# Kernel optimization log

Measured on AMD Instinct MI355X. Metric: run time of the kernel, lower is better.

Reference implementation:

```python
import jax, jax.numpy as jnp
import numpy as np

A_DIM = 18
HID = 512
LSTM_IN = HID + A_DIM + 1  # 531


def setup_inputs() -> dict:
    key = jax.random.key(0)
    ks = jax.random.split(key, 26)
    T, B = 80, 64
    inp = {}
    inp["o"] = jax.random.randint(ks[0], (T, B, 1, 84, 84), 0, 255, dtype=jnp.int32)
    inp["a"] = jax.random.randint(ks[1], (T, B), 0, A_DIM, dtype=jnp.int32)
    inp["r"] = jax.random.normal(ks[2], (T, B), dtype=jnp.float32)
    inp["done"] = jax.random.randint(ks[3], (T, B), 0, 2, dtype=jnp.int32)
    inp["h0"] = jnp.zeros((B, HID), dtype=jnp.float32)
    inp["c0"] = jnp.zeros((B, HID), dtype=jnp.float32)

    def gw(k, shape, s=0.05):
        return (jax.random.normal(k, shape, dtype=jnp.float32) * s)

    # CNN trunk params (torch Conv2d OIHW layout)
    inp["conv1_w"] = gw(ks[4], (32, 1, 8, 8))
    inp["conv1_b"] = jnp.zeros((32,), jnp.float32)
    inp["conv2_w"] = gw(ks[5], (64, 32, 4, 4))
    inp["conv2_b"] = jnp.zeros((64,), jnp.float32)
    inp["conv3_w"] = gw(ks[6], (64, 64, 3, 3))
    inp["conv3_b"] = jnp.zeros((64,), jnp.float32)
    inp["fc_w"] = gw(ks[7], (HID, 64 * 7 * 7))
    inp["fc_b"] = jnp.zeros((HID,), jnp.float32)
    # LSTM params (torch gate order: i, f, g, o)
    inp["W_ih"] = gw(ks[8], (4 * HID, LSTM_IN))
    inp["W_hh"] = gw(ks[9], (4 * HID, HID))
    inp["b_ih"] = jnp.zeros((4 * HID,), jnp.float32)
    inp["b_hh"] = jnp.zeros((4 * HID,), jnp.float32)
    # Dueling heads
    inp["adv_w1"] = gw(ks[10], (HID, HID))
    inp["adv_b1"] = jnp.zeros((HID,), jnp.float32)
    inp["adv_w2"] = gw(ks[11], (A_DIM, HID))
    inp["adv_b2"] = jnp.zeros((A_DIM,), jnp.float32)
    inp["val_w1"] = gw(ks[12], (HID, HID))
    inp["val_b1"] = jnp.zeros((HID,), jnp.float32)
    inp["val_w2"] = gw(ks[13], (1, HID))
    inp["val_b2"] = jnp.zeros((1,), jnp.float32)
    return inp


def _conv(x, w, b, stride):
    y = jax.lax.conv_general_dilated(
        x, w, (stride, stride), 'VALID',
        dimension_numbers=('NCHW', 'OIHW', 'NCHW'))
    return y + b[None, :, None, None]


def reference(o, a, r, done, h0, c0,
              conv1_w, conv1_b, conv2_w, conv2_b, conv3_w, conv3_b,
              fc_w, fc_b, W_ih, W_hh, b_ih, b_hh,
              adv_w1, adv_b1, adv_w2, adv_b2,
              val_w1, val_b1, val_w2, val_b2):
    T, B = o.shape[0], o.shape[1]
    x = o.reshape(T * B, 1, 84, 84).astype(jnp.float32) / 255.0
    x = jax.nn.relu(_conv(x, conv1_w, conv1_b, 4))   # [TB,32,20,20]
    x = jax.nn.relu(_conv(x, conv2_w, conv2_b, 2))   # [TB,64,9,9]
    x = jax.nn.relu(_conv(x, conv3_w, conv3_b, 1))   # [TB,64,7,7]
    x = x.reshape(T * B, 64 * 7 * 7)
    hidden = jax.nn.relu(x @ fc_w.T + fc_b).reshape(T, B, HID)

    a_one_hot = jax.nn.one_hot(a, A_DIM, dtype=jnp.float32)      # [T,B,A]
    lstm_in = jnp.concatenate([hidden, r[..., None], a_one_hot], axis=-1)  # [T,B,531]
    keep = (1.0 - done.astype(jnp.float32))[..., None]           # [T,B,1]
    bias = b_ih + b_hh

    def step(carry, inp_t):
        h, c = carry
        x_t, m = inp_t
        h = h * m
        c = c * m
        g = x_t @ W_ih.T + h @ W_hh.T + bias   # [B, 4H]
        i, f, gg, oo = jnp.split(g, 4, axis=-1)
        c = jax.nn.sigmoid(f) * c + jax.nn.sigmoid(i) * jnp.tanh(gg)
        h = jax.nn.sigmoid(oo) * jnp.tanh(c)
        return (h, c), h

    (hT, cT), hs = jax.lax.scan(step, (h0, c0), (lstm_in, keep))
    z = hs.reshape(T * B, HID)

    adv = jax.nn.relu(z @ adv_w1.T + adv_b1) @ adv_w2.T + adv_b2  # [TB,A]
    val = jax.nn.relu(z @ val_w1.T + val_b1) @ val_w2.T + val_b2  # [TB,1]
    q = val + (adv - adv.mean(axis=1, keepdims=True))
    return q.reshape(T, B, A_DIM), hT, cT
```

## Files before the change

### kernel.cpp

```cpp
#include <hip/hip_runtime.h>
#include <hip/hip_bf16.h>
#include <stdint.h>

typedef __bf16 bf16;
typedef __bf16 bfrag __attribute__((ext_vector_type(8)));
typedef short s16x8 __attribute__((ext_vector_type(8)));
typedef float f32x4 __attribute__((ext_vector_type(4)));
typedef float f32x16 __attribute__((ext_vector_type(16)));
typedef uint32_t u32x4 __attribute__((ext_vector_type(4)));

#define DEV __device__ __forceinline__

DEV bfrag ldg16(const bf16* p){ return *(const bfrag*)p; }

struct U64x2 { uint64_t a, b; };
DEV bfrag ld2x8(const bf16* p){
  U64x2 t; t.a = *(const uint64_t*)p; t.b = *(const uint64_t*)(p+4);
  return __builtin_bit_cast(bfrag, t);
}

DEV f32x4  mfma16(bfrag a, bfrag b, f32x4  c){ return __builtin_amdgcn_mfma_f32_16x16x32_bf16(a,b,c,0,0,0); }
DEV f32x16 mfma32(bfrag a, bfrag b, f32x16 c){ return __builtin_amdgcn_mfma_f32_32x32x16_bf16(a,b,c,0,0,0); }

DEV f32x16 zero16(){
  f32x16 v;
  for(int i=0;i<16;++i) v[i]=0.f;
  return v;
}
DEV f32x4 zero4(){
  f32x4 v;
  for(int i=0;i<4;++i) v[i]=0.f;
  return v;
}

DEV float sigm(float x){ return 1.0f/(1.0f+__expf(-x)); }
DEV float ftanh(float x){ float e = __expf(2.f*x); return 1.f - 2.f/(e+1.f); }

DEV u32x4 ldcg4(const uint32_t* p){
  u32x4 r;
  asm volatile("global_load_dwordx4 %0, %1, off sc0 sc1" : "=v"(r) : "v"(p));
  return r;
}

DEV uint32_t pkbf(uint32_t a, uint32_t b){
  bf16 x = (bf16)__builtin_bit_cast(float,a), y = (bf16)__builtin_bit_cast(float,b);
  return (uint32_t)__builtin_bit_cast(uint16_t,x) | ((uint32_t)__builtin_bit_cast(uint16_t,y)<<16);
}

__global__ __launch_bounds__(256) void k_prep(
    const float* __restrict__ c1w, const float* __restrict__ c2w,
    const float* __restrict__ c3w, const float* __restrict__ fcw,
    const float* __restrict__ Wih, const float* __restrict__ WhhF,
    const float* __restrict__ bih, const float* __restrict__ bhh,
    const float* __restrict__ aw1, const float* __restrict__ aw2,
    const float* __restrict__ vw1, const float* __restrict__ vw2,
    const float* __restrict__ h0,
    bf16* w1b, bf16* w2r, bf16* w3r, bf16* fcwr, bf16* Wx, bf16* Whh,
    float* biasL, float* Wr, float* Wa, bf16* headw1, float* headb1,
    bf16* w2cat, uint32_t* hcurT)
{
  long i = (long)blockIdx.x*256 + threadIdx.x;
  if (i < 2048){ int co=(int)(i>>6), k=(int)(i&63);
    w1b[i] = (bf16)(c1w[co*64+k]*(1.f/255.f)); return; } i -= 2048;
  if (i < 32768){ int o=(int)(i>>9), k=(int)(i&511);
    int ky=k>>7, kx=(k>>5)&3, ci=k&31;
    w2r[i] = (bf16)c2w[((o*32+ci)*4+ky)*4+kx]; return; } i -= 32768;
  if (i < 36864){ int o=(int)(i/576), k=(int)(i%576);
    int ky=k/192, rem=k-ky*192, kx=rem>>6, ci=rem&63;
    w3r[i] = (bf16)c3w[((o*64+ci)*3+ky)*3+kx]; return; } i -= 36864;
  if (i < 1638400){ int o=(int)(i/3200), k=(int)(i%3200);
    float v = 0.f;
    if (k < 3136){ int y=k/448, rem=k-y*448, x=rem>>6, ci=rem&63;
      v = fcw[o*3136 + ci*49 + y*7 + x]; }
    fcwr[i] = (bf16)v; return; } i -= 1638400;
  if (i < 1048576){ int n=(int)(i>>9), k=(int)(i&511);
    Wx[i] = (bf16)Wih[n*531+k]; return; } i -= 1048576;
  if (i < 1048576){ int n=(int)(i>>9), k=(int)(i&511);
    Whh[i] = (bf16)WhhF[n*512+k]; return; } i -= 1048576;
  if (i < 2048){ biasL[i] = bih[i]+bhh[i]; return; } i -= 2048;
  if (i < 2048){ Wr[i] = Wih[i*531+512]; return; } i -= 2048;
  if (i < 36864){ int j=(int)(i>>11), n=(int)(i&2047);
    Wa[i] = Wih[n*531+513+j]; return; } i -= 36864;
  if (i < 524288){ headw1[i] = (bf16)(i<262144 ? aw1[i] : vw1[i-262144]); return; } i -= 524288;
  if (i < 1024){ headb1[i] = 0.f; return; } i -= 1024;
  if (i < 32768){ int n=(int)(i>>10), k=(int)(i&1023);
    float v = 0.f;
    if (n<18 && k<512) v = aw2[n*512+k];
    else if (n==18 && k>=512) v = vw2[k-512];
    w2cat[i] = (bf16)v; return; } i -= 32768;
  if (i < 65536){
    if (i < 32768){
      uint32_t b = __builtin_bit_cast(uint32_t, h0[i]) & ~127u;
      hcurT[i] = b;
    } else {
      hcurT[i] = 0u;
    }
    return;
  }
}

__global__ __launch_bounds__(256) void k_prep2(
    const float* __restrict__ ab1, const float* __restrict__ vb1, float* headb1)
{
  int i = blockIdx.x*256 + threadIdx.x;
  headb1[i] = (i<512) ? ab1[i] : vb1[i-512];
}

__global__ __launch_bounds__(512,1) void k_conv12(
    const int* __restrict__ o, const bf16* __restrict__ w1b,
    const float* __restrict__ c1b, const bf16* __restrict__ w2r,
    const float* __restrict__ c2b, bf16* __restrict__ act2)
{
  __shared__ bf16 simg[4][7056];
  __shared__ bf16 lact[4][12800];
  const int tid = threadIdx.x;
  const long imgbase = (long)blockIdx.x*4;
  const int4* src = (const int4*)o;
  for (int u = tid; u < 7056; u += 512){
    int4 v = src[imgbase*1764 + u];
    int il = u/1764, p4 = u - il*1764;
    uint32_t lo = (uint32_t)__builtin_bit_cast(uint16_t,(bf16)(float)v.x)
                | ((uint32_t)__builtin_bit_cast(uint16_t,(bf16)(float)v.y)<<16);
    uint32_t hi = (uint32_t)__builtin_bit_cast(uint16_t,(bf16)(float)v.z)
                | ((uint32_t)__builtin_bit_cast(uint16_t,(bf16)(float)v.w)<<16);
    *(uint64_t*)&simg[il][p4*4] = (uint64_t)lo | ((uint64_t)hi<<32);
  }
  __syncthreads();
  const int w = tid>>6, l = tid&63;
  const int img = w>>1, h = w&1;
  const bf16* sp = &simg[img][0];
  char* lw = (char*)&lact[img][0];
  {
    bfrag bw[4];
    #pragma unroll
    for (int ks=0;ks<4;++ks) bw[ks] = ldg16(w1b + (l&31)*64 + ks*16 + 8*(l>>5));
    const float bias = c1b[l&31];
    for (int mt=h; mt<13; mt+=2){
      f32x16 acc = zero16();
      int m0 = mt*32 + (l&31);
      int p  = m0>399 ? 399 : m0;
      int oy = p/20, ox = p - oy*20;
      #pragma unroll
      for (int ks=0;ks<4;++ks){
        int ky = 2*ks + (l>>5);
        bfrag a = ld2x8(sp + (oy*4+ky)*84 + ox*4);
        acc = mfma32(a, bw[ks], acc);
      }
      #pragma unroll
      for (int r2=0;r2<16;++r2){
        int row = (r2&3) + 8*(r2>>2) + 4*(l>>5);
        int m = mt*32 + row;
        if (m < 400){
          float v = acc[r2] + bias; v = v>0.f ? v : 0.f;
          *(bf16*)(lw + m*64 + (((l&31)*2) ^ ((m&3)<<4))) = (bf16)v;
        }
      }
    }
  }
  __syncthreads();
  {
    f32x16 acc2[3];
    #pragma unroll
    for (int a2=0;a2<3;++a2) acc2[a2]=zero16();
    int pb[3];
    #pragma unroll
    for (int mt=0;mt<3;++mt){
      int m = mt*32 + (l&31); int p = m>80 ? 80 : m;
      int oy = p/9, ox = p - oy*9;
      pb[mt] = (oy*2)*20 + ox*2;
    }
    #pragma unroll 4
    for (int ks=0; ks<32; ++ks){
      int k  = ks*16 + 8*(l>>5);
      int ky = k>>7, kx = (k>>5)&3, ci = k&31;
      bfrag b0 = ldg16(w2r + (32*h + (l&31))*512 + k);
      #pragma unroll
      for (int mt=0; mt<3; ++mt){
        int p2 = pb[mt] + ky*20 + kx;
        bfrag a = *(const bfrag*)(lw + p2*64 + ((ci*2) ^ ((p2&3)<<4)));
        acc2[mt] = mfma32(a, b0, acc2[mt]);
      }
    }
    const float bias2 = c2b[32*h + (l&31)];
    #pragma unroll
    for (int mt=0; mt<3; ++mt){
      #pragma unroll
      for (int r2=0;r2<16;++r2){
        int row = (r2&3) + 8*(r2>>2) + 4*(l>>5);
        int m = mt*32 + row;
        if (m < 81){
          float v = acc2[mt][r2] + bias2; v = v>0.f ? v : 0.f;
          act2[(imgbase+img)*5184 + m*64 + 32*h + (l&31)] = (bf16)v;
        }
      }
    }
  }
}

__global__ __launch_bounds__(256,2) void k_conv3(
    const bf16* __restrict__ act2, const bf16* __restrict__ w3r,
    const float* __restrict__ c3b, bf16* __restrict__ act3)
{
  const int tid=threadIdx.x, w=tid>>6, l=tid&63;
  const long img = (long)blockIdx.x*4 + w;
  const bf16* A = act2 + img*5184;
  f32x16 acc[2][2];
  #pragma unroll
  for(int a2=0;a2<2;++a2){ acc[a2][0]=zero16(); acc[a2][1]=zero16(); }
  #pragma unroll 4
  for (int ks=0; ks<36; ++ks){
    int k  = ks*16 + 8*(l>>5);
    int ky = k/192, rem = k - ky*192, kx = rem>>6, ci = rem&63;
    bfrag b0 = ldg16(w3r + (l&31)*576 + k);
    bfrag b1 = ldg16(w3r + (32+(l&31))*576 + k);
    #pragma unroll
    for (int mt=0; mt<2; ++mt){
      int m = mt*32 + (l&31); int p = m>48 ? 48 : m;
      int oy = p/7, ox = p - oy*7;
      bfrag a = ldg16(A + ((oy+ky)*9 + (ox+kx))*64 + ci);
      acc[mt][0] = mfma32(a, b0, acc[mt][0]);
      acc[mt][1] = mfma32(a, b1, acc[mt][1]);
    }
  }
  const float bias0 = c3b[l&31], bias1 = c3b[32+(l&31)];
  #pragma unroll
  for (int mt=0; mt<2; ++mt){
    #pragma unroll
    for (int r2=0;r2<16;++r2){
      int row = (r2&3) + 8*(r2>>2) + 4*(l>>5);
      int m = mt*32 + row;
      if (m < 50){
        float v0 = 0.f, v1 = 0.f;
        if (m < 49){
          v0 = acc[mt][0][r2] + bias0; v0 = v0>0.f ? v0 : 0.f;
          v1 = acc[mt][1][r2] + bias1; v1 = v1>0.f ? v1 : 0.f;
        }
        act3[img*3200 + m*64 + (l&31)]      = (bf16)v0;
        act3[img*3200 + m*64 + 32 + (l&31)] = (bf16)v1;
      }
    }
  }
}

template<bool RELU, bool OUTBF16>
__global__ __launch_bounds__(256,4) void k_gemm(
    const bf16* __restrict__ A, long lda,
    const bf16* __restrict__ W, long ldb,
    const float* __restrict__ bias,
    float* __restrict__ outF, bf16* __restrict__ outB, long ldo, int K,
    const float* __restrict__ fixR, const int* __restrict__ fixA,
    const float* __restrict__ fixWr, const float* __restrict__ fixWa)
{
  __shared__ bf16 sA[8192];
  char* sb = (char*)sA;
  const int tid=threadIdx.x, w=tid>>6, l=tid&63;
  const int m0 = blockIdx.x*64, n0 = blockIdx.y*128;
  f32x16 acc[2]; acc[0]=zero16(); acc[1]=zero16();
  const int mt = w&1;
  const int rowa = mt*32 + (l&31);
  for (int kc=0; kc<K; kc+=128){
    __syncthreads();
    for (int u = tid; u < 1024; u += 256){
      int row = u>>4, seg = u&15;
      s16x8 v = *(const s16x8*)(A + (long)(m0+row)*lda + kc + seg*8);
      *(s16x8*)(sb + row*256 + ((seg*16) ^ ((row&15)<<4))) = v;
    }
    __syncthreads();
    #pragma unroll
    for (int ks=0; ks<8; ++ks){
      bfrag a = *(const bfrag*)(sb + rowa*256 + ((ks*32 + (l>>5)*16) ^ ((rowa&15)<<4)));
      #pragma unroll
      for (int j=0;j<2;++j){
        int nt = (w>>1)*2 + j;
        bfrag b = ldg16(W + (long)(n0 + nt*32 + (l&31))*ldb + kc + ks*16 + 8*(l>>5));
        acc[j] = mfma32(a, b, acc[j]);
      }
    }
  }
  #pragma unroll
  for (int j=0;j<2;++j){
    int nt = (w>>1)*2 + j;
    int gc = n0 + nt*32 + (l&31);
    float bv = bias ? bias[gc] : 0.f;
    float wrv = fixR ? fixWr[gc] : 0.f;
    #pragma unroll
    for (int r2=0;r2<16;++r2){
      int row = (r2&3) + 8*(r2>>2) + 4*(l>>5);
      long gr = m0 + mt*32 + row;
      float v = acc[j][r2] + bv;
      if (fixR) v += fixR[gr]*wrv + fixWa[(long)fixA[gr]*2048 + gc];
      if (RELU) v = v>0.f ? v : 0.f;
      if (OUTBF16) outB[gr*ldo + gc] = (bf16)v;
      else         outF[gr*ldo + gc] = v;
    }
  }
}

__global__ __launch_bounds__(256,1) void k_lstm(
    const float* __restrict__ G, const int* __restrict__ done,
    const float* __restrict__ c0, const bf16* __restrict__ Whh,
    uint32_t* __restrict__ hcurT, bf16* __restrict__ hseq,
    float* __restrict__ outH, float* __restrict__ outC)
{
  __shared__ bf16 swt[65536];
  __shared__ bf16 sh2[8192];
  __shared__ float sg[4][16][33];
  __shared__ float sc[16][33];
  __shared__ char  sdone[80][16];
  const int tid=threadIdx.x, w=tid>>6, l=tid&63;
  const int blk=blockIdx.x;
  const int grp=(blk&7)>>1, jj=((blk&1)<<3)|(blk>>3);
  const int bb = grp*16, uu = jj*32;

  for (int p=tid; p<512; p+=256){ int m=p>>5, u=p&31; sc[m][u] = c0[(bb+m)*512 + uu + u]; }
  for (int p=tid; p<1280; p+=256){ int t=p>>4, m=p&15; sdone[t][m] = (char)done[t*64 + bb + m]; }

  char* swb = (char*)swt;
  for (int u = tid; u < 8192; u += 256){
    int wg = u>>11, ks2 = (u>>6)&31, ll = u&63;
    int row = uu + (ll&15) + ((ks2&1)<<4);
    int k   = (ks2>>1)*32 + 8*(ll>>4);
    bfrag v = ldg16(Whh + ((long)wg*512 + row)*512 + k);
    *(bfrag*)(swb + ((u*16) ^ ((ks2&7)<<4))) = v;
  }

  char* shb = (char*)sh2;
  const char* wbase = swb + w*32768;
  const int loff = l*16;
  const int srow  = tid>>4;
  const int sci   = tid&15;

  __syncthreads();

  for (int t=0; t<80; ++t){
    float gv0[4], gv1[4];
    {
      const float* Gt = G + ((long)t*64 + bb)*2048 + w*512 + uu;
      #pragma unroll
      for (int r2=0;r2<4;++r2){
        int m2 = (l>>4)*4 + r2;
        gv0[r2] = Gt[(long)m2*2048 + (l&15)];
        gv1[r2] = Gt[(long)m2*2048 + 16 + (l&15)];
      }
    }
    __builtin_amdgcn_sched_barrier(0);
    {
      const uint32_t* hb = hcurT + (size_t)(t&1)*32768 + (size_t)(bb+srow)*512 + sci*32;
      u32x4 hv[8];
      const uint32_t exp = (uint32_t)t;
      for (;;){
        #pragma unroll
        for (int j2=0;j2<8;++j2) hv[j2] = ldcg4(hb + j2*4);
        asm volatile("s_waitcnt vmcnt(0)" ::: "memory");
        bool ok = true;
        #pragma unroll
        for (int j2=0;j2<8;++j2){
          ok &= ((hv[j2][0]&127u)==exp) & ((hv[j2][1]&127u)==exp)
              & ((hv[j2][2]&127u)==exp) & ((hv[j2][3]&127u)==exp);
        }
        if (__all(ok)) break;
      }
      if (sdone[t][srow]){
        #pragma unroll
        for (int j2=0;j2<8;++j2){ u32x4 z = {0,0,0,0}; hv[j2] = z; }
      }
      #pragma unroll
      for (int j=0;j<4;++j){
        u32x4 outp;
        outp[0] = pkbf(hv[2*j][0],   hv[2*j][1]);
        outp[1] = pkbf(hv[2*j][2],   hv[2*j][3]);
        outp[2] = pkbf(hv[2*j+1][0], hv[2*j+1][1]);
        outp[3] = pkbf(hv[2*j+1][2], hv[2*j+1][3]);
        *(u32x4*)(shb + sci*1024 + ((((srow + 16*j)*16)) ^ ((sci&7)<<4))) = outp;
      }
    }
    __syncthreads();
    f32x4 a0e = zero4(), a0o = zero4(), a1e = zero4(), a1o = zero4();
    #pragma unroll
    for (int ks=0; ks<16; ++ks){
      bfrag a  = *(const bfrag*)(shb + ks*1024 + (loff ^ ((ks&7)<<4)));
      bfrag b0 = *(const bfrag*)(wbase + (2*ks)*1024   + (loff ^ (((2*ks)&7)<<4)));
      bfrag b1 = *(const bfrag*)(wbase + (2*ks+1)*1024 + (loff ^ (((2*ks+1)&7)<<4)));
      if (ks & 1){ a0o = mfma16(a, b0, a0o); a1o = mfma16(a, b1, a1o); }
      else       { a0e = mfma16(a, b0, a0e); a1e = mfma16(a, b1, a1e); }
    }
    #pragma unroll
    for (int r2=0;r2<4;++r2){
      int m = (l>>4)*4 + r2;
      sg[w][m][(l&15)]    = a0e[r2] + a0o[r2] + gv0[r2];
      sg[w][m][16+(l&15)] = a1e[r2] + a1o[r2] + gv1[r2];
    }
    __syncthreads();
    {
      int p0 = tid*2; int m = p0>>5, u = p0&31;
      int dn = sdone[t][m];
      float c_0 = dn ? 0.f : sc[m][u];
      float c_1 = dn ? 0.f : sc[m][u+1];
      float i0=sg[0][m][u],   f0=sg[1][m][u],   g0=sg[2][m][u],   o0=sg[3][m][u];
      float i1=sg[0][m][u+1], f1=sg[1][m][u+1], g1=sg[2][m][u+1], o1=sg[3][m][u+1];
      float cn0 = sigm(f0)*c_0 + sigm(i0)*ftanh(g0);
      float cn1 = sigm(f1)*c_1 + sigm(i1)*ftanh(g1);
      float h_0 = sigm(o0)*ftanh(cn0);
      float h_1 = sigm(o1)*ftanh(cn1);
      sc[m][u] = cn0; sc[m][u+1] = cn1;
      uint32_t tb0 = (__builtin_bit_cast(uint32_t, h_0) & ~127u) | (uint32_t)(t+1);
      uint32_t tb1 = (__builtin_bit_cast(uint32_t, h_1) & ~127u) | (uint32_t)(t+1);
      uint64_t pk64 = (uint64_t)tb0 | ((uint64_t)tb1<<32);
      __hip_atomic_store(
          (uint64_t*)(hcurT + (size_t)((t+1)&1)*32768 + (size_t)(bb+m)*512 + uu + u),
          pk64, __ATOMIC_RELAXED, __HIP_MEMORY_SCOPE_AGENT);
      uint32_t pk = (uint32_t)__builtin_bit_cast(uint16_t,(bf16)h_0)
                  | ((uint32_t)__builtin_bit_cast(uint16_t,(bf16)h_1)<<16);
      *(uint32_t*)(hseq + ((long)t*64 + bb + m)*512 + uu + u) = pk;
      if (t == 79){
        outH[(bb+m)*512 + uu + u]   = h_0;  outH[(bb+m)*512 + uu + u+1] = h_1;
        outC[(bb+m)*512 + uu + u]   = cn0;  outC[(bb+m)*512 + uu + u+1] = cn1;
      }
    }
  }
}

__global__ __launch_bounds__(256) void k_qhead(
    const bf16* __restrict__ zav, const bf16* __restrict__ w2cat,
    const float* __restrict__ ab2, const float* __restrict__ vb2,
    float* __restrict__ q)
{
  __shared__ float sq[4][16][33];
  const int tid=threadIdx.x, w=tid>>6, l=tid&63;
  const int s0 = blockIdx.x*64 + w*16;
  f32x4 acc0 = zero4(), acc1 = zero4();
  const int row = l&15;
  #pragma unroll 4
  for (int ks=0; ks<32; ++ks){
    int k = ks*32 + 8*(l>>4);
    bfrag a  = ldg16(zav + (long)(s0+row)*1024 + k);
    bfrag b0 = ldg16(w2cat + (l&15)*1024 + k);
    bfrag b1 = ldg16(w2cat + (16+(l&15))*1024 + k);
    acc0 = mfma16(a, b0, acc0);
    acc1 = mfma16(a, b1, acc1);
  }
  #pragma unroll
  for (int r2=0;r2<4;++r2){
    int m = (l>>4)*4 + r2;
    sq[w][m][l&15]      = acc0[r2];
    sq[w][m][16+(l&15)] = acc1[r2];
  }
  __syncthreads();
  if (l < 16){
    int s = s0 + l;
    float av[18]; float sum = 0.f;
    #pragma unroll
    for (int j=0;j<18;++j){ av[j] = sq[w][l][j] + ab2[j]; sum += av[j]; }
    float val = sq[w][l][18] + vb2[0];
    float mean = sum * (1.f/18.f);
    #pragma unroll
    for (int j=0;j<18;++j) q[(long)s*18 + j] = val + av[j] - mean;
  }
}

extern "C" void kernel_launch(void* const* d_in, const int* in_sizes, int n_in,
                              void* d_out, int out_size, void* d_ws, size_t ws_size,
                              hipStream_t stream)
{
  (void)in_sizes; (void)n_in; (void)out_size;
  const int*   o_in = (const int*)  d_in[0];
  const int*   a_in = (const int*)  d_in[1];
  const float* r_in = (const float*)d_in[2];
  const int*   done = (const int*)  d_in[3];
  const float* h0   = (const float*)d_in[4];
  const float* c0   = (const float*)d_in[5];
  const float* c1w  = (const float*)d_in[6],  *c1b=(const float*)d_in[7];
  const float* c2w  = (const float*)d_in[8],  *c2b=(const float*)d_in[9];
  const float* c3w  = (const float*)d_in[10], *c3b=(const float*)d_in[11];
  const float* fcw  = (const float*)d_in[12], *fcb=(const float*)d_in[13];
  const float* Wih  = (const float*)d_in[14], *WhhF=(const float*)d_in[15];
  const float* bih  = (const float*)d_in[16], *bhh=(const float*)d_in[17];
  const float* aw1  = (const float*)d_in[18], *ab1=(const float*)d_in[19];
  const float* aw2  = (const float*)d_in[20], *ab2=(const float*)d_in[21];
  const float* vw1  = (const float*)d_in[22], *vb1=(const float*)d_in[23];
  const float* vw2  = (const float*)d_in[24], *vb2=(const float*)d_in[25];

  char* ws = (char*)d_ws;
  size_t off = 0;
  auto alloc = [&](size_t b){ size_t p = off; off = (off + b + 255) & ~(size_t)255; return p; };
  bf16*  act2   = (bf16*) (ws + alloc(53084160));
  bf16*  act3   = (bf16*) (ws + alloc(32768000));
  bf16*  hidden = (bf16*) (ws + alloc(5242880));
  uint32_t* hcurT = (uint32_t*)(ws + alloc(262144));
  bf16*  w1b    = (bf16*) (ws + alloc(4096));
  bf16*  w2r    = (bf16*) (ws + alloc(65536));
  bf16*  w3r    = (bf16*) (ws + alloc(73728));
  bf16*  fcwr   = (bf16*) (ws + alloc(3276800));
  bf16*  Wx     = (bf16*) (ws + alloc(2097152));
  bf16*  Whh    = (bf16*) (ws + alloc(2097152));
  float* biasL  = (float*)(ws + alloc(8192));
  float* Wr     = (float*)(ws + alloc(8192));
  float* Wa     = (float*)(ws + alloc(147456));
  bf16*  headw1 = (bf16*) (ws + alloc(1048576));
  float* headb1 = (float*)(ws + alloc(4096));
  bf16*  w2cat  = (bf16*) (ws + alloc(65536));
  if (off > ws_size) return;

  float* G    = (float*)act2;
  bf16*  hseq = hidden;
  bf16*  zav  = act3;

  float* qout = (float*)d_out;
  float* outH = qout + 92160;
  float* outC = qout + 124928;

  k_prep<<<17468, 256, 0, stream>>>(c1w, c2w, c3w, fcw, Wih, WhhF, bih, bhh,
      aw1, aw2, vw1, vw2, h0, w1b, w2r, w3r, fcwr, Wx, Whh,
      biasL, Wr, Wa, headw1, headb1, w2cat, hcurT);
  k_prep2<<<4, 256, 0, stream>>>(ab1, vb1, headb1);

  k_conv12<<<1280, 512, 0, stream>>>(o_in, w1b, c1b, w2r, c2b, act2);
  k_conv3<<<1280, 256, 0, stream>>>(act2, w3r, c3b, act3);
  k_gemm<true,true><<<dim3(80,4), 256, 0, stream>>>(
      act3, 3200, fcwr, 3200, fcb, nullptr, hidden, 512, 3200,
      nullptr, nullptr, nullptr, nullptr);
  k_gemm<false,false><<<dim3(80,16), 256, 0, stream>>>(
      hidden, 512, Wx, 512, biasL, G, nullptr, 2048, 512,
      r_in, a_in, Wr, Wa);

  k_lstm<<<64, 256, 0, stream>>>(G, done, c0, Whh, hcurT, hseq, outH, outC);

  k_gemm<true,true><<<dim3(80,8), 256, 0, stream>>>(
      hseq, 512, headw1, 512, headb1, nullptr, zav, 1024, 512,
      nullptr, nullptr, nullptr, nullptr);
  k_qhead<<<80, 256, 0, stream>>>(zav, w2cat, ab2, vb2, qout);
}
```

Before: 738.0 us.

## Exchange LSTM hidden state as packed bf16 with 2-bit step tags

The cross-block hidden-state exchange buffer moves from fp32 words with a 7-bit step tag to packed bf16 pairs. A 2-bit step phase is stored in the low mantissa bit of each bf16 half. This halves the bytes each block polls and publishes per timestep and removes the fp32-to-bf16 repacking on the read side. The polling loop also adds s_sleep between retries. In exchange, one extra mantissa bit of h is lost, and correctness now depends on a 4-phase tag that wraps.

After: 653.0 us. 1.13x faster.

```diff
diff --git a/kernel.cpp b/kernel.cpp
--- a/kernel.cpp
+++ b/kernel.cpp
@@ -42,8 +42,8 @@
   return r;
 }
 
-DEV uint32_t pkbf(uint32_t a, uint32_t b){
-  bf16 x = (bf16)__builtin_bit_cast(float,a), y = (bf16)__builtin_bit_cast(float,b);
+DEV uint32_t pk2f(float a, float b){
+  bf16 x = (bf16)a, y = (bf16)b;
   return (uint32_t)__builtin_bit_cast(uint16_t,x) | ((uint32_t)__builtin_bit_cast(uint16_t,y)<<16);
 }
 
@@ -88,12 +88,13 @@
     if (n<18 && k<512) v = aw2[n*512+k];
     else if (n==18 && k>=512) v = vw2[k-512];
     w2cat[i] = (bf16)v; return; } i -= 32768;
-  if (i < 65536){
-    if (i < 32768){
-      uint32_t b = __builtin_bit_cast(uint32_t, h0[i]) & ~127u;
-      hcurT[i] = b;
+  if (i < 32768){
+    if (i < 16384){
+      int row = (int)(i>>8), wd = (int)(i&255);
+      uint32_t pk = pk2f(h0[row*512 + wd*2], h0[row*512 + wd*2 + 1]);
+      hcurT[i] = pk & ~0x00010001u;
     } else {
-      hcurT[i] = 0u;
+      hcurT[i] = 0x00010000u;
     }
     return;
   }
@@ -345,33 +346,35 @@
     }
     __builtin_amdgcn_sched_barrier(0);
     {
-      const uint32_t* hb = hcurT + (size_t)(t&1)*32768 + (size_t)(bb+srow)*512 + sci*32;
-      u32x4 hv[8];
-      const uint32_t exp = (uint32_t)t;
+      const uint32_t* hb = hcurT + (size_t)(t&1)*16384 + (size_t)(bb+srow)*256 + sci*16;
+      u32x4 hv[4];
+      const uint32_t expPat = ((uint32_t)(t&1)) | (((uint32_t)((t>>1)&1))<<16);
       for (;;){
         #pragma unroll
-        for (int j2=0;j2<8;++j2) hv[j2] = ldcg4(hb + j2*4);
+        for (int j2=0;j2<4;++j2) hv[j2] = ldcg4(hb + j2*4);
         asm volatile("s_waitcnt vmcnt(0)" ::: "memory");
         bool ok = true;
         #pragma unroll
-        for (int j2=0;j2<8;++j2){
-          ok &= ((hv[j2][0]&127u)==exp) & ((hv[j2][1]&127u)==exp)
-              & ((hv[j2][2]&127u)==exp) & ((hv[j2][3]&127u)==exp);
+        for (int j2=0;j2<4;++j2){
+          ok &= ((hv[j2][0]&0x00010001u)==expPat) & ((hv[j2][1]&0x00010001u)==expPat)
+              & ((hv[j2][2]&0x00010001u)==expPat) & ((hv[j2][3]&0x00010001u)==expPat);
         }
         if (__all(ok)) break;
+        __builtin_amdgcn_s_sleep(1);
       }
       if (sdone[t][srow]){
         #pragma unroll
-        for (int j2=0;j2<8;++j2){ u32x4 z = {0,0,0,0}; hv[j2] = z; }
+        for (int j2=0;j2<4;++j2){ u32x4 z = {0,0,0,0}; hv[j2] = z; }
+      } else {
+        #pragma unroll
+        for (int j2=0;j2<4;++j2){
+          hv[j2][0] &= ~0x00010001u; hv[j2][1] &= ~0x00010001u;
+          hv[j2][2] &= ~0x00010001u; hv[j2][3] &= ~0x00010001u;
+        }
       }
       #pragma unroll
       for (int j=0;j<4;++j){
-        u32x4 outp;
-        outp[0] = pkbf(hv[2*j][0],   hv[2*j][1]);
-        outp[1] = pkbf(hv[2*j][2],   hv[2*j][3]);
-        outp[2] = pkbf(hv[2*j+1][0], hv[2*j+1][1]);
-        outp[3] = pkbf(hv[2*j+1][2], hv[2*j+1][3]);
-        *(u32x4*)(shb + sci*1024 + ((((srow + 16*j)*16)) ^ ((sci&7)<<4))) = outp;
+        *(u32x4*)(shb + sci*1024 + ((((srow + 16*j)*16)) ^ ((sci&7)<<4))) = hv[j];
       }
     }
     __syncthreads();
@@ -403,14 +406,13 @@
       float h_0 = sigm(o0)*ftanh(cn0);
       float h_1 = sigm(o1)*ftanh(cn1);
       sc[m][u] = cn0; sc[m][u+1] = cn1;
-      uint32_t tb0 = (__builtin_bit_cast(uint32_t, h_0) & ~127u) | (uint32_t)(t+1);
-      uint32_t tb1 = (__builtin_bit_cast(uint32_t, h_1) & ~127u) | (uint32_t)(t+1);
-      uint64_t pk64 = (uint64_t)tb0 | ((uint64_t)tb1<<32);
+      uint32_t pk = pk2f(h_0, h_1);
+      int p1 = (t+1)&3;
+      uint32_t pat = ((uint32_t)(p1&1)) | (((uint32_t)(p1>>1))<<16);
+      uint32_t pkT = (pk & ~0x00010001u) | pat;
       __hip_atomic_store(
-          (uint64_t*)(hcurT + (size_t)((t+1)&1)*32768 + (size_t)(bb+m)*512 + uu + u),
-          pk64, __ATOMIC_RELAXED, __HIP_MEMORY_SCOPE_AGENT);
-      uint32_t pk = (uint32_t)__builtin_bit_cast(uint16_t,(bf16)h_0)
-                  | ((uint32_t)__builtin_bit_cast(uint16_t,(bf16)h_1)<<16);
+          hcurT + (size_t)((t+1)&1)*16384 + (size_t)(bb+m)*256 + ((uu+u)>>1),
+          pkT, __ATOMIC_RELAXED, __HIP_MEMORY_SCOPE_AGENT);
       *(uint32_t*)(hseq + ((long)t*64 + bb + m)*512 + uu + u) = pk;
       if (t == 79){
         outH[(bb+m)*512 + uu + u]   = h_0;  outH[(bb+m)*512 + uu + u+1] = h_1;
@@ -486,7 +488,7 @@
   bf16*  act2   = (bf16*) (ws + alloc(53084160));
   bf16*  act3   = (bf16*) (ws + alloc(32768000));
   bf16*  hidden = (bf16*) (ws + alloc(5242880));
-  uint32_t* hcurT = (uint32_t*)(ws + alloc(262144));
+  uint32_t* hcurT = (uint32_t*)(ws + alloc(131072));
   bf16*  w1b    = (bf16*) (ws + alloc(4096));
   bf16*  w2r    = (bf16*) (ws + alloc(65536));
   bf16*  w3r    = (bf16*) (ws + alloc(73728));
@@ -509,7 +511,7 @@
   float* outH = qout + 92160;
   float* outC = qout + 124928;
 
-  k_prep<<<17468, 256, 0, stream>>>(c1w, c2w, c3w, fcw, Wih, WhhF, bih, bhh,
+  k_prep<<<17340, 256, 0, stream>>>(c1w, c2w, c3w, fcw, Wih, WhhF, bih, bhh,
       aw1, aw2, vw1, vw2, h0, w1b, w2r, w3r, fcwr, Wx, Whh,
       biasL, Wr, Wa, headw1, headb1, w2cat, hcurT);
   k_prep2<<<4, 256, 0, stream>>>(ab1, vb1, headb1);
```
